# Performance work log

Hardware: AMD Instinct MI355X
Metric: run time of the kernel (lower is better)

Reference implementation:

```python
import jax, jax.numpy as jnp
import numpy as np

IMG_SIZE = 8192
VAR = (0.1, 0.2)          # cfg['variance']
CONF_THRES = 0.9
IOU_THRES = 0.5
TOP_K = 4096              # fixed pre-NMS cap (jit-able replacement for dynamic nonzero/nms sizes)
MIN_SIZES = [[16, 32], [64, 128], [256, 512]]
STEPS = [8, 16, 32]


def _priorbox():
    # Faithful reimplementation of priorbox(min_sizes, steps, clip=False, image_size=(S,S)),
    # vectorized: per cell the anchors for each min_size are interleaved, as in the loop version.
    anchors = []
    for k, step in enumerate(STEPS):
        f = int(np.ceil(IMG_SIZE / step))
        ys, xs = np.meshgrid(np.arange(f, dtype=np.float32), np.arange(f, dtype=np.float32), indexing='ij')
        cx = (xs + 0.5) * step / IMG_SIZE
        cy = (ys + 0.5) * step / IMG_SIZE
        per_size = []
        for m in MIN_SIZES[k]:
            s = np.float32(m / IMG_SIZE)
            per_size.append(np.stack([cx, cy, np.full_like(cx, s), np.full_like(cx, s)], axis=-1))
        anchors.append(np.stack(per_size, axis=2).reshape(-1, 4))  # [f, f, n_sizes, 4] -> [f*f*n_sizes, 4]
    return np.concatenate(anchors, axis=0).astype(np.float32)


def setup_inputs() -> dict:
    key = jax.random.key(0)
    k1, k2, k3 = jax.random.split(key, 3)
    priors = jnp.asarray(_priorbox())                    # [N, 4] (cx, cy, s, s)
    N = priors.shape[0]                                  # 2,752,512
    loc = jax.random.normal(k1, (N, 4), jnp.float32)
    conf = jax.random.uniform(k2, (N, 2), jnp.float32)   # post-softmax class scores
    landm = jax.random.normal(k3, (N, 10), jnp.float32)  # 5 landmark deltas
    return {"loc": loc, "conf": conf, "landm": landm, "priors": priors}


def _decode_boxes(loc, priors):
    # decode(): center-size deltas -> corner boxes (x1, y1, x2, y2)
    xy = priors[:, :2] + loc[:, :2] * VAR[0] * priors[:, 2:]
    wh = priors[:, 2:] * jnp.exp(loc[:, 2:] * VAR[1])
    return jnp.concatenate([xy - 0.5 * wh, xy + 0.5 * wh], axis=1)


def _decode_landm(landm, priors):
    pts = landm.reshape(-1, 5, 2)
    pts = priors[:, None, :2] + pts * VAR[0] * priors[:, None, 2:]
    return pts.reshape(-1, 10)


def _iou_matrix(b):
    # b: [K, 4] corner boxes -> pairwise IoU [K, K]
    area = jnp.clip(b[:, 2] - b[:, 0], 0.0) * jnp.clip(b[:, 3] - b[:, 1], 0.0)
    lt = jnp.maximum(b[:, None, :2], b[None, :, :2])
    rb = jnp.minimum(b[:, None, 2:], b[None, :, 2:])
    wh = jnp.clip(rb - lt, 0.0)
    inter = wh[..., 0] * wh[..., 1]
    return inter / (area[:, None] + area[None, :] - inter + 1e-12)


def reference(loc, conf, landm, priors):
    boxes = _decode_boxes(loc, priors) * IMG_SIZE        # [N, 4]
    landmarks = _decode_landm(landm, priors) * IMG_SIZE  # [N, 10]
    scores = conf[:, 1]                                  # [N]

    # score threshold + fixed-size top-k (jit-able analogue of nonzero(scores > thres))
    masked = jnp.where(scores > CONF_THRES, scores, -jnp.inf)
    top_s, top_i = jax.lax.top_k(masked, TOP_K)          # sorted descending, as torchvision.ops.nms expects
    valid = top_s > CONF_THRES

    b = boxes[top_i]                                     # [K, 4]
    s = scores[top_i]                                    # [K]
    lm = landmarks[top_i]                                # [K, 10]

    # greedy NMS: boxes are score-sorted; suppress later boxes with IoU > thres vs any kept earlier box
    iou = _iou_matrix(b)                                 # [K, K]
    idx = jnp.arange(TOP_K)

    def body(i, keep):
        suppress = keep[i] & (iou[i] > IOU_THRES) & (idx > i)
        return keep & ~suppress

    keep = jax.lax.fori_loop(0, TOP_K, body, valid)

    out = jnp.concatenate([b, s[:, None], lm], axis=1)   # [K, 15] = boxes | score | landmarks
    # zero padded/suppressed rows (fixed-shape stand-in for dynamic boxes[keep])
    return out * keep[:, None].astype(out.dtype)
```

## Files before the change

kernel.cpp:

```cpp
#include <hip/hip_runtime.h>
#include <stdint.h>

typedef unsigned long long u64;
typedef unsigned int u32;

#define CONF_T 0.9f
#define IOU_T 0.5f
#define TOPK 4096
#define CAP 384

#define BINCNT_OFF 0
#define VALIDW_OFF 16384
#define NZW_OFF    16896
#define SELBOX_OFF 32768
#define SELSC_OFF  98304
#define SELLM_OFF  114688
#define MASK_OFF   278528
#define BINSEG_OFF 2375680

__device__ __forceinline__ int score_bin(float s) {
    u32 b = __float_as_uint(s);
    if (b >= 0x3F800000u) return 0;
    int bin = (int)((0x3F800000u - b) >> 9);
    return bin > 4095 ? 4095 : bin;
}

__global__ void k_zero(u32* __restrict__ binCnt, u64* __restrict__ validw,
                       u64* __restrict__ nzw) {
    int i = blockIdx.x * 256 + threadIdx.x;
    binCnt[i] = 0u;
    if (i < 64) { validw[i] = 0ull; nzw[i] = 0ull; }
}

__global__ void __launch_bounds__(256) k_compact(
        const float4* __restrict__ conf4, int N2,
        u32* __restrict__ binCnt, u64* __restrict__ binseg) {
    int stride = gridDim.x * 256;
    for (int i = blockIdx.x * 256 + threadIdx.x; i < N2; i += stride) {
        float4 v = conf4[i];
        if (v.y > CONF_T) {
            int b = score_bin(v.y);
            u32 p = atomicAdd(&binCnt[b], 1u);
            if (p < CAP)
                binseg[(size_t)b * CAP + p] =
                    ((u64)__float_as_uint(v.y) << 32) | (u64)(~(u32)(2 * i));
        }
        if (v.w > CONF_T) {
            int b = score_bin(v.w);
            u32 p = atomicAdd(&binCnt[b], 1u);
            if (p < CAP)
                binseg[(size_t)b * CAP + p] =
                    ((u64)__float_as_uint(v.w) << 32) | (u64)(~(u32)(2 * i + 1));
        }
    }
}

__global__ void __launch_bounds__(256) k_rankscan(
        const float4* __restrict__ loc, const float4* __restrict__ priors,
        const float* __restrict__ landm, const u32* __restrict__ binCnt,
        const u64* __restrict__ binseg,
        float4* __restrict__ selbox, float* __restrict__ selscore,
        float* __restrict__ sellm) {
    __shared__ u32 pref_s[4097];
    __shared__ u32 parts[256];
    __shared__ u32 m_sh;
    int t = threadIdx.x;
    u32 h[16];
    u32 sum = 0;
    #pragma unroll
    for (int i = 0; i < 16; i++) {
        u32 c = binCnt[t * 16 + i];
        h[i] = c > CAP ? CAP : c;
        sum += h[i];
    }
    parts[t] = sum;
    if (t == 0) m_sh = 0u;
    __syncthreads();
    for (int d = 1; d < 256; d <<= 1) {
        u32 add = (t >= d) ? parts[t - d] : 0u;
        __syncthreads();
        parts[t] += add;
        __syncthreads();
    }
    u32 incl = parts[t];
    u32 excl = incl - sum;
    u32 run = excl;
    #pragma unroll
    for (int i = 0; i < 16; i++) { pref_s[t * 16 + i] = run; run += h[i]; }
    if (t == 255) pref_s[4096] = run;
    __syncthreads();
    u32 total = pref_s[4096];
    u32 target = total < TOPK ? total : TOPK;
    if (total > 0 && excl < target && incl >= target) {
        u32 r2 = excl;
        #pragma unroll
        for (int i = 0; i < 16; i++) {
            r2 += h[i];
            if (r2 >= target) { m_sh = r2; break; }
        }
    }
    __syncthreads();
    u32 M = m_sh;
    u32 p = blockIdx.x * 256 + t;
    if (p >= M) {
        if (p < TOPK) {
            selbox[p] = make_float4(0.f, 0.f, 0.f, 0.f);
            selscore[p] = 0.f;
            #pragma unroll
            for (int q = 0; q < 10; q++) sellm[(size_t)p * 10 + q] = 0.f;
        }
        return;
    }
    int lo = 0, hi = 4095;
    while (lo < hi) {
        int mid = (lo + hi + 1) >> 1;
        if (pref_s[mid] <= p) lo = mid; else hi = mid - 1;
    }
    u32 st = pref_s[lo];
    u32 cnt = pref_s[lo + 1] - st;
    const u64* seg = binseg + (size_t)lo * CAP;
    u64 key = seg[p - st];
    u32 rank = st;
    for (u32 j = 0; j < cnt; j++) rank += (seg[j] > key) ? 1u : 0u;
    if (rank >= TOPK) return;
    u32 idx = ~(u32)key;
    float sc = __uint_as_float((u32)(key >> 32));
    float4 L = loc[idx];
    float4 P = priors[idx];
    float cx = P.x + L.x * 0.1f * P.z;
    float cy = P.y + L.y * 0.1f * P.w;
    float wx = P.z * expf(L.z * 0.2f);
    float wy = P.w * expf(L.w * 0.2f);
    float4 bx;
    bx.x = (cx - 0.5f * wx) * 8192.f;
    bx.y = (cy - 0.5f * wy) * 8192.f;
    bx.z = (cx + 0.5f * wx) * 8192.f;
    bx.w = (cy + 0.5f * wy) * 8192.f;
    selbox[rank] = bx;
    selscore[rank] = sc;
    const float* lmr = landm + (size_t)idx * 10;
    float* lmo = sellm + (size_t)rank * 10;
    #pragma unroll
    for (int q = 0; q < 5; q++) {
        float lx = lmr[2 * q], ly = lmr[2 * q + 1];
        lmo[2 * q]     = (P.x + lx * 0.1f * P.z) * 8192.f;
        lmo[2 * q + 1] = (P.y + ly * 0.1f * P.w) * 8192.f;
    }
}

__global__ void __launch_bounds__(256) k_maskout(
        const float4* __restrict__ selbox, const float* __restrict__ selscore,
        const float* __restrict__ sellm,
        u64* __restrict__ mask, u64* __restrict__ validw, u64* __restrict__ nzw,
        float* __restrict__ out) {
    __shared__ float4 sb[TOPK];
    int t = threadIdx.x, b = blockIdx.x;
    for (int i = t; i < TOPK; i += 256) sb[i] = selbox[i];
    __syncthreads();
    int wv = t >> 6, lane = t & 63;
    int rbase = b * 16 + wv * 4;
    float4 r0 = sb[rbase], r1 = sb[rbase + 1], r2 = sb[rbase + 2], r3 = sb[rbase + 3];
    float a0 = fmaxf(r0.z - r0.x, 0.f) * fmaxf(r0.w - r0.y, 0.f);
    float a1 = fmaxf(r1.z - r1.x, 0.f) * fmaxf(r1.w - r1.y, 0.f);
    float a2 = fmaxf(r2.z - r2.x, 0.f) * fmaxf(r2.w - r2.y, 0.f);
    float a3 = fmaxf(r3.z - r3.x, 0.f) * fmaxf(r3.w - r3.y, 0.f);
    u64 w0 = 0, w1 = 0, w2 = 0, w3 = 0;
    for (int w = 0; w < 64; w++) {
        if (w * 64 + 63 <= rbase) continue;
        int j = w * 64 + lane;
        float4 bj = sb[j];
        float aj = fmaxf(bj.z - bj.x, 0.f) * fmaxf(bj.w - bj.y, 0.f);
        #define IOU_BIT(rr, aa, row) ({ \
            float lx = fmaxf(rr.x, bj.x), ly = fmaxf(rr.y, bj.y); \
            float rx = fminf(rr.z, bj.z), ry = fminf(rr.w, bj.w); \
            float inter = fmaxf(rx - lx, 0.f) * fmaxf(ry - ly, 0.f); \
            float iou = inter / (aa + aj - inter + 1e-12f); \
            (j > (row)) && (iou > IOU_T); })
        u64 bb0 = __ballot(IOU_BIT(r0, a0, rbase + 0));
        u64 bb1 = __ballot(IOU_BIT(r1, a1, rbase + 1));
        u64 bb2 = __ballot(IOU_BIT(r2, a2, rbase + 2));
        u64 bb3 = __ballot(IOU_BIT(r3, a3, rbase + 3));
        #undef IOU_BIT
        if (lane == w) { w0 = bb0; w1 = bb1; w2 = bb2; w3 = bb3; }
    }
    mask[(size_t)(rbase + 0) * 64 + lane] = w0;
    mask[(size_t)(rbase + 1) * 64 + lane] = w1;
    mask[(size_t)(rbase + 2) * 64 + lane] = w2;
    mask[(size_t)(rbase + 3) * 64 + lane] = w3;
    u64 nz0 = __ballot(w0 != 0ull), nz1 = __ballot(w1 != 0ull);
    u64 nz2 = __ballot(w2 != 0ull), nz3 = __ballot(w3 != 0ull);
    u64 vb = __ballot(lane < 4 && selscore[rbase + lane] > CONF_T);
    if (lane == 0) {
        int g = rbase >> 6;
        int sh = rbase & 63;
        u64 nzb = (nz0 ? 1ull : 0) | (nz1 ? 2ull : 0) | (nz2 ? 4ull : 0) | (nz3 ? 8ull : 0);
        if (vb)  atomicOr(&validw[g], vb << sh);
        if (nzb) atomicOr(&nzw[g], nzb << sh);
    }
    if (t < 240) {
        int row = b * 16 + t / 15;
        int col = t - (t / 15) * 15;
        const float* sbf = (const float*)selbox;
        float val;
        if (col < 4)       val = sbf[row * 4 + col];
        else if (col == 4) val = selscore[row];
        else               val = sellm[(size_t)row * 10 + (col - 5)];
        out[(size_t)row * 15 + col] = val;
    }
}

__global__ void __launch_bounds__(1024) k_nmszero(
        const u64* __restrict__ mask, const u64* __restrict__ validw_arr,
        const u64* __restrict__ nzw_arr, float* __restrict__ out) {
    __shared__ u64 keep_s[64];
    int tid = threadIdx.x;
    if (tid < 64) {
        int t = tid;
        u64 vw = validw_arr[t];
        u64 nzv = nzw_arr[t];
        u64 sup = 0ull, keepw = 0ull;
        for (int g = 0; g < 64; g++) {
            u64 cur = __shfl(sup, g);
            u64 validg = __shfl(vw, g);
            u64 nzg = __shfl(nzv, g);
            u64 alive = (~cur) & validg;
            if (nzg) {
                u64 intra = mask[(size_t)(g * 64 + t) * 64 + g];
                u64 rem = nzg;
                while (rem) {
                    int bb = __ffsll((long long)rem) - 1;
                    rem &= rem - 1;
                    if ((alive >> bb) & 1ull) {
                        u64 rowb = __shfl(intra, bb);
                        alive &= ~rowb;
                    }
                }
            }
            if (t == g) keepw = alive;
            u64 srem = alive & nzg;
            const u64* mb = mask + (size_t)(g * 64) * 64 + t;
            while (srem) {
                int i0, i1 = -1, i2 = -1, i3 = -1, i4 = -1, i5 = -1, i6 = -1, i7 = -1;
                i0 = __ffsll((long long)srem) - 1; srem &= srem - 1;
                if (srem) { i1 = __ffsll((long long)srem) - 1; srem &= srem - 1;
                if (srem) { i2 = __ffsll((long long)srem) - 1; srem &= srem - 1;
                if (srem) { i3 = __ffsll((long long)srem) - 1; srem &= srem - 1;
                if (srem) { i4 = __ffsll((long long)srem) - 1; srem &= srem - 1;
                if (srem) { i5 = __ffsll((long long)srem) - 1; srem &= srem - 1;
                if (srem) { i6 = __ffsll((long long)srem) - 1; srem &= srem - 1;
                if (srem) { i7 = __ffsll((long long)srem) - 1; srem &= srem - 1; } } } } } } }
                u64 a0 = mb[(size_t)i0 * 64];
                u64 a1 = (i1 >= 0) ? mb[(size_t)i1 * 64] : 0ull;
                u64 a2 = (i2 >= 0) ? mb[(size_t)i2 * 64] : 0ull;
                u64 a3 = (i3 >= 0) ? mb[(size_t)i3 * 64] : 0ull;
                u64 a4 = (i4 >= 0) ? mb[(size_t)i4 * 64] : 0ull;
                u64 a5 = (i5 >= 0) ? mb[(size_t)i5 * 64] : 0ull;
                u64 a6 = (i6 >= 0) ? mb[(size_t)i6 * 64] : 0ull;
                u64 a7 = (i7 >= 0) ? mb[(size_t)i7 * 64] : 0ull;
                sup |= (a0 | a1) | (a2 | a3) | ((a4 | a5) | (a6 | a7));
            }
        }
        keep_s[t] = keepw;
    }
    __syncthreads();
    for (int r = tid; r < TOPK; r += 1024) {
        if (!((keep_s[r >> 6] >> (r & 63)) & 1ull)) {
            float* o = out + (size_t)r * 15;
            #pragma unroll
            for (int q = 0; q < 15; q++) o[q] = 0.f;
        }
    }
}

extern "C" void kernel_launch(void* const* d_in, const int* in_sizes, int n_in,
                              void* d_out, int out_size, void* d_ws, size_t ws_size,
                              hipStream_t stream) {
    const float4* loc    = (const float4*)d_in[0];
    const float4* conf4  = (const float4*)d_in[1];
    const float*  landm  = (const float*)d_in[2];
    const float4* priors = (const float4*)d_in[3];
    float* out = (float*)d_out;
    int N = in_sizes[1] / 2;
    int N2 = N / 2;

    char* ws = (char*)d_ws;
    u32* binCnt   = (u32*)(ws + BINCNT_OFF);
    u64* validw   = (u64*)(ws + VALIDW_OFF);
    u64* nzw      = (u64*)(ws + NZW_OFF);
    float4* selbox = (float4*)(ws + SELBOX_OFF);
    float* selsc   = (float*)(ws + SELSC_OFF);
    float* sellm   = (float*)(ws + SELLM_OFF);
    u64* maskp    = (u64*)(ws + MASK_OFF);
    u64* binseg   = (u64*)(ws + BINSEG_OFF);

    k_zero<<<16, 256, 0, stream>>>(binCnt, validw, nzw);
    k_compact<<<1024, 256, 0, stream>>>(conf4, N2, binCnt, binseg);
    k_rankscan<<<32, 256, 0, stream>>>(loc, priors, landm, binCnt, binseg,
                                       selbox, selsc, sellm);
    k_maskout<<<256, 256, 0, stream>>>(selbox, selsc, sellm, maskp, validw, nzw, out);
    k_nmszero<<<1, 1024, 0, stream>>>(maskp, validw, nzw, out);
}
```

Before: 97.42 us.

## Fuse NMS pipeline into one cooperative persistent kernel with grid syncs

Replaces the five separate kernel launches (zero, compact, rankscan, maskout, nmszero) with a single cooperative kernel of 512 blocks that separates the stages with grid.sync(). The intent is to remove launch gaps and inter-kernel dependency overhead. The IoU mask stage now gives each block 8 rows instead of 16, and the final output is written once, masked by a keep bitmap in global memory, rather than written and then partly zeroed. In exchange it adds five grid-wide barriers and 64 KB of static shared memory per block, which limits occupancy during the memory-bound compaction scan.

```diff
diff --git a/kernel.cpp b/kernel.cpp
--- a/kernel.cpp
+++ b/kernel.cpp
@@ -1,5 +1,8 @@
 #include <hip/hip_runtime.h>
+#include <hip/hip_cooperative_groups.h>
 #include <stdint.h>
+
+namespace cg = cooperative_groups;
 
 typedef unsigned long long u64;
 typedef unsigned int u32;
@@ -8,10 +11,14 @@
 #define IOU_T 0.5f
 #define TOPK 4096
 #define CAP 384
+#define NB 512
+#define NT 256
+#define NTOT (NB * NT)
 
 #define BINCNT_OFF 0
 #define VALIDW_OFF 16384
 #define NZW_OFF    16896
+#define KEEPG_OFF  17408
 #define SELBOX_OFF 32768
 #define SELSC_OFF  98304
 #define SELLM_OFF  114688
@@ -25,199 +32,175 @@
     return bin > 4095 ? 4095 : bin;
 }
 
-__global__ void k_zero(u32* __restrict__ binCnt, u64* __restrict__ validw,
-                       u64* __restrict__ nzw) {
-    int i = blockIdx.x * 256 + threadIdx.x;
-    binCnt[i] = 0u;
-    if (i < 64) { validw[i] = 0ull; nzw[i] = 0ull; }
-}
-
-__global__ void __launch_bounds__(256) k_compact(
+__global__ void __launch_bounds__(NT) mega(
         const float4* __restrict__ conf4, int N2,
-        u32* __restrict__ binCnt, u64* __restrict__ binseg) {
-    int stride = gridDim.x * 256;
-    for (int i = blockIdx.x * 256 + threadIdx.x; i < N2; i += stride) {
+        const float4* __restrict__ loc, const float4* __restrict__ priors,
+        const float* __restrict__ landm,
+        u32* __restrict__ binCnt, u64* __restrict__ binseg,
+        float4* __restrict__ selbox, float* __restrict__ selscore,
+        float* __restrict__ sellm,
+        u64* __restrict__ mask, u64* __restrict__ validw, u64* __restrict__ nzw,
+        u64* __restrict__ keepg, float* __restrict__ out) {
+    cg::grid_group grid = cg::this_grid();
+    __shared__ alignas(16) char smem[65536];
+    int t = threadIdx.x, b = blockIdx.x;
+    int gtid = b * NT + t;
+
+    if (gtid < 4096) binCnt[gtid] = 0u;
+    if (gtid < 64) { validw[gtid] = 0ull; nzw[gtid] = 0ull; }
+    grid.sync();
+
+    for (int i = gtid; i < N2; i += NTOT) {
         float4 v = conf4[i];
         if (v.y > CONF_T) {
-            int b = score_bin(v.y);
-            u32 p = atomicAdd(&binCnt[b], 1u);
+            int bb = score_bin(v.y);
+            u32 p = atomicAdd(&binCnt[bb], 1u);
             if (p < CAP)
-                binseg[(size_t)b * CAP + p] =
+                binseg[(size_t)bb * CAP + p] =
                     ((u64)__float_as_uint(v.y) << 32) | (u64)(~(u32)(2 * i));
         }
         if (v.w > CONF_T) {
-            int b = score_bin(v.w);
-            u32 p = atomicAdd(&binCnt[b], 1u);
+            int bb = score_bin(v.w);
+            u32 p = atomicAdd(&binCnt[bb], 1u);
             if (p < CAP)
-                binseg[(size_t)b * CAP + p] =
+                binseg[(size_t)bb * CAP + p] =
                     ((u64)__float_as_uint(v.w) << 32) | (u64)(~(u32)(2 * i + 1));
         }
     }
-}
-
-__global__ void __launch_bounds__(256) k_rankscan(
-        const float4* __restrict__ loc, const float4* __restrict__ priors,
-        const float* __restrict__ landm, const u32* __restrict__ binCnt,
-        const u64* __restrict__ binseg,
-        float4* __restrict__ selbox, float* __restrict__ selscore,
-        float* __restrict__ sellm) {
-    __shared__ u32 pref_s[4097];
-    __shared__ u32 parts[256];
-    __shared__ u32 m_sh;
-    int t = threadIdx.x;
-    u32 h[16];
-    u32 sum = 0;
-    #pragma unroll
-    for (int i = 0; i < 16; i++) {
-        u32 c = binCnt[t * 16 + i];
-        h[i] = c > CAP ? CAP : c;
-        sum += h[i];
-    }
-    parts[t] = sum;
-    if (t == 0) m_sh = 0u;
-    __syncthreads();
-    for (int d = 1; d < 256; d <<= 1) {
-        u32 add = (t >= d) ? parts[t - d] : 0u;
-        __syncthreads();
-        parts[t] += add;
-        __syncthreads();
-    }
-    u32 incl = parts[t];
-    u32 excl = incl - sum;
-    u32 run = excl;
-    #pragma unroll
-    for (int i = 0; i < 16; i++) { pref_s[t * 16 + i] = run; run += h[i]; }
-    if (t == 255) pref_s[4096] = run;
-    __syncthreads();
-    u32 total = pref_s[4096];
-    u32 target = total < TOPK ? total : TOPK;
-    if (total > 0 && excl < target && incl >= target) {
-        u32 r2 = excl;
+    grid.sync();
+
+    if (b < 32) {
+        u32* pref_s = (u32*)smem;
+        u32* parts  = (u32*)(smem + 16400);
+        u32* m_sh   = (u32*)(smem + 17424);
+        u32 h[16];
+        u32 sum = 0;
         #pragma unroll
         for (int i = 0; i < 16; i++) {
-            r2 += h[i];
-            if (r2 >= target) { m_sh = r2; break; }
-        }
-    }
-    __syncthreads();
-    u32 M = m_sh;
-    u32 p = blockIdx.x * 256 + t;
-    if (p >= M) {
-        if (p < TOPK) {
-            selbox[p] = make_float4(0.f, 0.f, 0.f, 0.f);
-            selscore[p] = 0.f;
+            u32 c = binCnt[t * 16 + i];
+            h[i] = c > CAP ? CAP : c;
+            sum += h[i];
+        }
+        parts[t] = sum;
+        if (t == 0) *m_sh = 0u;
+        __syncthreads();
+        for (int d = 1; d < 256; d <<= 1) {
+            u32 add = (t >= d) ? parts[t - d] : 0u;
+            __syncthreads();
+            parts[t] += add;
+            __syncthreads();
+        }
+        u32 incl = parts[t];
+        u32 excl = incl - sum;
+        u32 run = excl;
+        #pragma unroll
+        for (int i = 0; i < 16; i++) { pref_s[t * 16 + i] = run; run += h[i]; }
+        if (t == 255) pref_s[4096] = run;
+        __syncthreads();
+        u32 total = pref_s[4096];
+        u32 target = total < TOPK ? total : TOPK;
+        if (total > 0 && excl < target && incl >= target) {
+            u32 r2 = excl;
             #pragma unroll
-            for (int q = 0; q < 10; q++) sellm[(size_t)p * 10 + q] = 0.f;
-        }
-        return;
-    }
-    int lo = 0, hi = 4095;
-    while (lo < hi) {
-        int mid = (lo + hi + 1) >> 1;
-        if (pref_s[mid] <= p) lo = mid; else hi = mid - 1;
-    }
-    u32 st = pref_s[lo];
-    u32 cnt = pref_s[lo + 1] - st;
-    const u64* seg = binseg + (size_t)lo * CAP;
-    u64 key = seg[p - st];
-    u32 rank = st;
-    for (u32 j = 0; j < cnt; j++) rank += (seg[j] > key) ? 1u : 0u;
-    if (rank >= TOPK) return;
-    u32 idx = ~(u32)key;
-    float sc = __uint_as_float((u32)(key >> 32));
-    float4 L = loc[idx];
-    float4 P = priors[idx];
-    float cx = P.x + L.x * 0.1f * P.z;
-    float cy = P.y + L.y * 0.1f * P.w;
-    float wx = P.z * expf(L.z * 0.2f);
-    float wy = P.w * expf(L.w * 0.2f);
-    float4 bx;
-    bx.x = (cx - 0.5f * wx) * 8192.f;
-    bx.y = (cy - 0.5f * wy) * 8192.f;
-    bx.z = (cx + 0.5f * wx) * 8192.f;
-    bx.w = (cy + 0.5f * wy) * 8192.f;
-    selbox[rank] = bx;
-    selscore[rank] = sc;
-    const float* lmr = landm + (size_t)idx * 10;
-    float* lmo = sellm + (size_t)rank * 10;
-    #pragma unroll
-    for (int q = 0; q < 5; q++) {
-        float lx = lmr[2 * q], ly = lmr[2 * q + 1];
-        lmo[2 * q]     = (P.x + lx * 0.1f * P.z) * 8192.f;
-        lmo[2 * q + 1] = (P.y + ly * 0.1f * P.w) * 8192.f;
-    }
-}
-
-__global__ void __launch_bounds__(256) k_maskout(
-        const float4* __restrict__ selbox, const float* __restrict__ selscore,
-        const float* __restrict__ sellm,
-        u64* __restrict__ mask, u64* __restrict__ validw, u64* __restrict__ nzw,
-        float* __restrict__ out) {
-    __shared__ float4 sb[TOPK];
-    int t = threadIdx.x, b = blockIdx.x;
-    for (int i = t; i < TOPK; i += 256) sb[i] = selbox[i];
-    __syncthreads();
-    int wv = t >> 6, lane = t & 63;
-    int rbase = b * 16 + wv * 4;
-    float4 r0 = sb[rbase], r1 = sb[rbase + 1], r2 = sb[rbase + 2], r3 = sb[rbase + 3];
-    float a0 = fmaxf(r0.z - r0.x, 0.f) * fmaxf(r0.w - r0.y, 0.f);
-    float a1 = fmaxf(r1.z - r1.x, 0.f) * fmaxf(r1.w - r1.y, 0.f);
-    float a2 = fmaxf(r2.z - r2.x, 0.f) * fmaxf(r2.w - r2.y, 0.f);
-    float a3 = fmaxf(r3.z - r3.x, 0.f) * fmaxf(r3.w - r3.y, 0.f);
-    u64 w0 = 0, w1 = 0, w2 = 0, w3 = 0;
-    for (int w = 0; w < 64; w++) {
-        if (w * 64 + 63 <= rbase) continue;
-        int j = w * 64 + lane;
-        float4 bj = sb[j];
-        float aj = fmaxf(bj.z - bj.x, 0.f) * fmaxf(bj.w - bj.y, 0.f);
-        #define IOU_BIT(rr, aa, row) ({ \
-            float lx = fmaxf(rr.x, bj.x), ly = fmaxf(rr.y, bj.y); \
-            float rx = fminf(rr.z, bj.z), ry = fminf(rr.w, bj.w); \
-            float inter = fmaxf(rx - lx, 0.f) * fmaxf(ry - ly, 0.f); \
-            float iou = inter / (aa + aj - inter + 1e-12f); \
-            (j > (row)) && (iou > IOU_T); })
-        u64 bb0 = __ballot(IOU_BIT(r0, a0, rbase + 0));
-        u64 bb1 = __ballot(IOU_BIT(r1, a1, rbase + 1));
-        u64 bb2 = __ballot(IOU_BIT(r2, a2, rbase + 2));
-        u64 bb3 = __ballot(IOU_BIT(r3, a3, rbase + 3));
-        #undef IOU_BIT
-        if (lane == w) { w0 = bb0; w1 = bb1; w2 = bb2; w3 = bb3; }
-    }
-    mask[(size_t)(rbase + 0) * 64 + lane] = w0;
-    mask[(size_t)(rbase + 1) * 64 + lane] = w1;
-    mask[(size_t)(rbase + 2) * 64 + lane] = w2;
-    mask[(size_t)(rbase + 3) * 64 + lane] = w3;
-    u64 nz0 = __ballot(w0 != 0ull), nz1 = __ballot(w1 != 0ull);
-    u64 nz2 = __ballot(w2 != 0ull), nz3 = __ballot(w3 != 0ull);
-    u64 vb = __ballot(lane < 4 && selscore[rbase + lane] > CONF_T);
-    if (lane == 0) {
-        int g = rbase >> 6;
-        int sh = rbase & 63;
-        u64 nzb = (nz0 ? 1ull : 0) | (nz1 ? 2ull : 0) | (nz2 ? 4ull : 0) | (nz3 ? 8ull : 0);
-        if (vb)  atomicOr(&validw[g], vb << sh);
-        if (nzb) atomicOr(&nzw[g], nzb << sh);
-    }
-    if (t < 240) {
-        int row = b * 16 + t / 15;
-        int col = t - (t / 15) * 15;
-        const float* sbf = (const float*)selbox;
-        float val;
-        if (col < 4)       val = sbf[row * 4 + col];
-        else if (col == 4) val = selscore[row];
-        else               val = sellm[(size_t)row * 10 + (col - 5)];
-        out[(size_t)row * 15 + col] = val;
-    }
-}
-
-__global__ void __launch_bounds__(1024) k_nmszero(
-        const u64* __restrict__ mask, const u64* __restrict__ validw_arr,
-        const u64* __restrict__ nzw_arr, float* __restrict__ out) {
-    __shared__ u64 keep_s[64];
-    int tid = threadIdx.x;
-    if (tid < 64) {
-        int t = tid;
-        u64 vw = validw_arr[t];
-        u64 nzv = nzw_arr[t];
+            for (int i = 0; i < 16; i++) {
+                r2 += h[i];
+                if (r2 >= target) { *m_sh = r2; break; }
+            }
+        }
+        __syncthreads();
+        u32 M = *m_sh;
+        u32 p = (u32)gtid;
+        if (p >= M) {
+            if (p < TOPK) {
+                selbox[p] = make_float4(0.f, 0.f, 0.f, 0.f);
+                selscore[p] = 0.f;
+                #pragma unroll
+                for (int q = 0; q < 10; q++) sellm[(size_t)p * 10 + q] = 0.f;
+            }
+        } else {
+            int lo = 0, hi = 4095;
+            while (lo < hi) {
+                int mid = (lo + hi + 1) >> 1;
+                if (pref_s[mid] <= p) lo = mid; else hi = mid - 1;
+            }
+            u32 st = pref_s[lo];
+            u32 cnt = pref_s[lo + 1] - st;
+            const u64* seg = binseg + (size_t)lo * CAP;
+            u64 key = seg[p - st];
+            u32 rank = st;
+            for (u32 j = 0; j < cnt; j++) rank += (seg[j] > key) ? 1u : 0u;
+            if (rank < TOPK) {
+                u32 idx = ~(u32)key;
+                float sc = __uint_as_float((u32)(key >> 32));
+                float4 L = loc[idx];
+                float4 P = priors[idx];
+                float cx = P.x + L.x * 0.1f * P.z;
+                float cy = P.y + L.y * 0.1f * P.w;
+                float wx = P.z * expf(L.z * 0.2f);
+                float wy = P.w * expf(L.w * 0.2f);
+                float4 bx;
+                bx.x = (cx - 0.5f * wx) * 8192.f;
+                bx.y = (cy - 0.5f * wy) * 8192.f;
+                bx.z = (cx + 0.5f * wx) * 8192.f;
+                bx.w = (cy + 0.5f * wy) * 8192.f;
+                selbox[rank] = bx;
+                selscore[rank] = sc;
+                const float* lmr = landm + (size_t)idx * 10;
+                float* lmo = sellm + (size_t)rank * 10;
+                #pragma unroll
+                for (int q = 0; q < 5; q++) {
+                    float lx = lmr[2 * q], ly = lmr[2 * q + 1];
+                    lmo[2 * q]     = (P.x + lx * 0.1f * P.z) * 8192.f;
+                    lmo[2 * q + 1] = (P.y + ly * 0.1f * P.w) * 8192.f;
+                }
+            }
+        }
+    }
+    grid.sync();
+
+    {
+        float4* sb = (float4*)smem;
+        for (int i = t; i < TOPK; i += NT) sb[i] = selbox[i];
+        __syncthreads();
+        int wv = t >> 6, lane = t & 63;
+        int rbase = b * 8 + wv * 2;
+        float4 r0 = sb[rbase], r1 = sb[rbase + 1];
+        float a0 = fmaxf(r0.z - r0.x, 0.f) * fmaxf(r0.w - r0.y, 0.f);
+        float a1 = fmaxf(r1.z - r1.x, 0.f) * fmaxf(r1.w - r1.y, 0.f);
+        u64 w0 = 0, w1 = 0;
+        for (int w = 0; w < 64; w++) {
+            if (w * 64 + 63 <= rbase) continue;
+            int j = w * 64 + lane;
+            float4 bj = sb[j];
+            float aj = fmaxf(bj.z - bj.x, 0.f) * fmaxf(bj.w - bj.y, 0.f);
+            #define IOU_BIT(rr, aa, row) ({ \
+                float lx = fmaxf(rr.x, bj.x), ly = fmaxf(rr.y, bj.y); \
+                float rx = fminf(rr.z, bj.z), ry = fminf(rr.w, bj.w); \
+                float inter = fmaxf(rx - lx, 0.f) * fmaxf(ry - ly, 0.f); \
+                float iou = inter / (aa + aj - inter + 1e-12f); \
+                (j > (row)) && (iou > IOU_T); })
+            u64 bb0 = __ballot(IOU_BIT(r0, a0, rbase + 0));
+            u64 bb1 = __ballot(IOU_BIT(r1, a1, rbase + 1));
+            #undef IOU_BIT
+            if (lane == w) { w0 = bb0; w1 = bb1; }
+        }
+        mask[(size_t)(rbase + 0) * 64 + lane] = w0;
+        mask[(size_t)(rbase + 1) * 64 + lane] = w1;
+        u64 nz0 = __ballot(w0 != 0ull), nz1 = __ballot(w1 != 0ull);
+        u64 vb = __ballot(lane < 2 && selscore[rbase + lane] > CONF_T);
+        if (lane == 0) {
+            int g = rbase >> 6;
+            int sh = rbase & 63;
+            u64 nzb = (nz0 ? 1ull : 0) | (nz1 ? 2ull : 0);
+            if (vb)  atomicOr(&validw[g], vb << sh);
+            if (nzb) atomicOr(&nzw[g], nzb << sh);
+        }
+    }
+    grid.sync();
+
+    if (b == 0 && t < 64) {
+        u64 vw = validw[t];
+        u64 nzv = nzw[t];
         u64 sup = 0ull, keepw = 0ull;
         for (int g = 0; g < 64; g++) {
             u64 cur = __shfl(sup, g);
@@ -260,15 +243,20 @@
                 sup |= (a0 | a1) | (a2 | a3) | ((a4 | a5) | (a6 | a7));
             }
         }
-        keep_s[t] = keepw;
-    }
-    __syncthreads();
-    for (int r = tid; r < TOPK; r += 1024) {
-        if (!((keep_s[r >> 6] >> (r & 63)) & 1ull)) {
-            float* o = out + (size_t)r * 15;
-            #pragma unroll
-            for (int q = 0; q < 15; q++) o[q] = 0.f;
-        }
+        keepg[t] = keepw;
+    }
+    grid.sync();
+
+    if (gtid < TOPK * 15) {
+        int row = gtid / 15;
+        int col = gtid - row * 15;
+        bool kp = (keepg[row >> 6] >> (row & 63)) & 1ull;
+        const float* sbf = (const float*)selbox;
+        float val;
+        if (col < 4)       val = sbf[row * 4 + col];
+        else if (col == 4) val = selscore[row];
+        else               val = sellm[(size_t)row * 10 + (col - 5)];
+        out[gtid] = kp ? val : 0.f;
     }
 }
 
@@ -287,16 +275,16 @@
     u32* binCnt   = (u32*)(ws + BINCNT_OFF);
     u64* validw   = (u64*)(ws + VALIDW_OFF);
     u64* nzw      = (u64*)(ws + NZW_OFF);
+    u64* keepg    = (u64*)(ws + KEEPG_OFF);
     float4* selbox = (float4*)(ws + SELBOX_OFF);
     float* selsc   = (float*)(ws + SELSC_OFF);
     float* sellm   = (float*)(ws + SELLM_OFF);
     u64* maskp    = (u64*)(ws + MASK_OFF);
     u64* binseg   = (u64*)(ws + BINSEG_OFF);
 
-    k_zero<<<16, 256, 0, stream>>>(binCnt, validw, nzw);
-    k_compact<<<1024, 256, 0, stream>>>(conf4, N2, binCnt, binseg);
-    k_rankscan<<<32, 256, 0, stream>>>(loc, priors, landm, binCnt, binseg,
-                                       selbox, selsc, sellm);
-    k_maskout<<<256, 256, 0, stream>>>(selbox, selsc, sellm, maskp, validw, nzw, out);
-    k_nmszero<<<1, 1024, 0, stream>>>(maskp, validw, nzw, out);
+    void* args[] = { &conf4, &N2, &loc, &priors, &landm,
+                     &binCnt, &binseg, &selbox, &selsc, &sellm,
+                     &maskp, &validw, &nzw, &keepg, &out };
+    hipLaunchCooperativeKernel(reinterpret_cast<void*>(mega),
+                               dim3(NB), dim3(NT), args, 0, stream);
 }
```

Measured after the change: 330.0 us. 3.39x slower.

## Balance IoU mask rows across waves and write output rows in rankscan

Applied to the files above, without the earlier changes.

Each wave in the mask kernel now takes four rows spread across the triangle (wid, 2047-wid, 2048+wid, 4095-wid), so every wave does about the same amount of upper-triangular IoU work. Before, consecutive rows gave early blocks much more work than late ones. The 15-float output rows are now written directly in the rankscan kernel, which removes the gather-and-copy step from the mask kernel. The NMS kernel is launched with 256 threads instead of 1024. The trade-off is that four dependent row passes now run per wave, with less instruction-level parallelism than the previous four-row interleaved ballots.

```diff
diff --git a/kernel.cpp b/kernel.cpp
--- a/kernel.cpp
+++ b/kernel.cpp
@@ -60,7 +60,7 @@
         const float* __restrict__ landm, const u32* __restrict__ binCnt,
         const u64* __restrict__ binseg,
         float4* __restrict__ selbox, float* __restrict__ selscore,
-        float* __restrict__ sellm) {
+        float* __restrict__ sellm, float* __restrict__ out) {
     __shared__ u32 pref_s[4097];
     __shared__ u32 parts[256];
     __shared__ u32 m_sh;
@@ -108,6 +108,9 @@
             selscore[p] = 0.f;
             #pragma unroll
             for (int q = 0; q < 10; q++) sellm[(size_t)p * 10 + q] = 0.f;
+            float* o = out + (size_t)p * 15;
+            #pragma unroll
+            for (int q = 0; q < 15; q++) o[q] = 0.f;
         }
         return;
     }
@@ -140,76 +143,59 @@
     selscore[rank] = sc;
     const float* lmr = landm + (size_t)idx * 10;
     float* lmo = sellm + (size_t)rank * 10;
+    float* o = out + (size_t)rank * 15;
+    o[0] = bx.x; o[1] = bx.y; o[2] = bx.z; o[3] = bx.w; o[4] = sc;
     #pragma unroll
     for (int q = 0; q < 5; q++) {
         float lx = lmr[2 * q], ly = lmr[2 * q + 1];
-        lmo[2 * q]     = (P.x + lx * 0.1f * P.z) * 8192.f;
-        lmo[2 * q + 1] = (P.y + ly * 0.1f * P.w) * 8192.f;
-    }
-}
-
-__global__ void __launch_bounds__(256) k_maskout(
+        float ox = (P.x + lx * 0.1f * P.z) * 8192.f;
+        float oy = (P.y + ly * 0.1f * P.w) * 8192.f;
+        lmo[2 * q] = ox; lmo[2 * q + 1] = oy;
+        o[5 + 2 * q] = ox; o[6 + 2 * q] = oy;
+    }
+}
+
+__global__ void __launch_bounds__(256) k_maskbal(
         const float4* __restrict__ selbox, const float* __restrict__ selscore,
-        const float* __restrict__ sellm,
-        u64* __restrict__ mask, u64* __restrict__ validw, u64* __restrict__ nzw,
-        float* __restrict__ out) {
+        u64* __restrict__ mask, u64* __restrict__ validw, u64* __restrict__ nzw) {
     __shared__ float4 sb[TOPK];
     int t = threadIdx.x, b = blockIdx.x;
     for (int i = t; i < TOPK; i += 256) sb[i] = selbox[i];
     __syncthreads();
     int wv = t >> 6, lane = t & 63;
-    int rbase = b * 16 + wv * 4;
-    float4 r0 = sb[rbase], r1 = sb[rbase + 1], r2 = sb[rbase + 2], r3 = sb[rbase + 3];
-    float a0 = fmaxf(r0.z - r0.x, 0.f) * fmaxf(r0.w - r0.y, 0.f);
-    float a1 = fmaxf(r1.z - r1.x, 0.f) * fmaxf(r1.w - r1.y, 0.f);
-    float a2 = fmaxf(r2.z - r2.x, 0.f) * fmaxf(r2.w - r2.y, 0.f);
-    float a3 = fmaxf(r3.z - r3.x, 0.f) * fmaxf(r3.w - r3.y, 0.f);
-    u64 w0 = 0, w1 = 0, w2 = 0, w3 = 0;
-    for (int w = 0; w < 64; w++) {
-        if (w * 64 + 63 <= rbase) continue;
-        int j = w * 64 + lane;
-        float4 bj = sb[j];
-        float aj = fmaxf(bj.z - bj.x, 0.f) * fmaxf(bj.w - bj.y, 0.f);
-        #define IOU_BIT(rr, aa, row) ({ \
-            float lx = fmaxf(rr.x, bj.x), ly = fmaxf(rr.y, bj.y); \
-            float rx = fminf(rr.z, bj.z), ry = fminf(rr.w, bj.w); \
-            float inter = fmaxf(rx - lx, 0.f) * fmaxf(ry - ly, 0.f); \
-            float iou = inter / (aa + aj - inter + 1e-12f); \
-            (j > (row)) && (iou > IOU_T); })
-        u64 bb0 = __ballot(IOU_BIT(r0, a0, rbase + 0));
-        u64 bb1 = __ballot(IOU_BIT(r1, a1, rbase + 1));
-        u64 bb2 = __ballot(IOU_BIT(r2, a2, rbase + 2));
-        u64 bb3 = __ballot(IOU_BIT(r3, a3, rbase + 3));
-        #undef IOU_BIT
-        if (lane == w) { w0 = bb0; w1 = bb1; w2 = bb2; w3 = bb3; }
-    }
-    mask[(size_t)(rbase + 0) * 64 + lane] = w0;
-    mask[(size_t)(rbase + 1) * 64 + lane] = w1;
-    mask[(size_t)(rbase + 2) * 64 + lane] = w2;
-    mask[(size_t)(rbase + 3) * 64 + lane] = w3;
-    u64 nz0 = __ballot(w0 != 0ull), nz1 = __ballot(w1 != 0ull);
-    u64 nz2 = __ballot(w2 != 0ull), nz3 = __ballot(w3 != 0ull);
-    u64 vb = __ballot(lane < 4 && selscore[rbase + lane] > CONF_T);
-    if (lane == 0) {
-        int g = rbase >> 6;
-        int sh = rbase & 63;
-        u64 nzb = (nz0 ? 1ull : 0) | (nz1 ? 2ull : 0) | (nz2 ? 4ull : 0) | (nz3 ? 8ull : 0);
-        if (vb)  atomicOr(&validw[g], vb << sh);
-        if (nzb) atomicOr(&nzw[g], nzb << sh);
-    }
-    if (t < 240) {
-        int row = b * 16 + t / 15;
-        int col = t - (t / 15) * 15;
-        const float* sbf = (const float*)selbox;
-        float val;
-        if (col < 4)       val = sbf[row * 4 + col];
-        else if (col == 4) val = selscore[row];
-        else               val = sellm[(size_t)row * 10 + (col - 5)];
-        out[(size_t)row * 15 + col] = val;
-    }
-}
-
-__global__ void __launch_bounds__(1024) k_nmszero(
+    int wid = b * 4 + wv;
+    int rows[4] = { wid, 2047 - wid, 2048 + wid, 4095 - wid };
+    #pragma unroll
+    for (int q = 0; q < 4; q++) {
+        int row = rows[q];
+        float4 ri = sb[row];
+        float ai = fmaxf(ri.z - ri.x, 0.f) * fmaxf(ri.w - ri.y, 0.f);
+        u64 myword = 0ull;
+        int wstart = row >> 6;
+        for (int w = wstart; w < 64; w++) {
+            int j = w * 64 + lane;
+            float4 bj = sb[j];
+            float aj = fmaxf(bj.z - bj.x, 0.f) * fmaxf(bj.w - bj.y, 0.f);
+            float lx = fmaxf(ri.x, bj.x), ly = fmaxf(ri.y, bj.y);
+            float rx = fminf(ri.z, bj.z), ry = fminf(ri.w, bj.w);
+            float inter = fmaxf(rx - lx, 0.f) * fmaxf(ry - ly, 0.f);
+            float iou = inter / (ai + aj - inter + 1e-12f);
+            bool pred = (j > row) && (iou > IOU_T);
+            u64 bb = __ballot(pred);
+            if (lane == w) myword = bb;
+        }
+        mask[(size_t)row * 64 + lane] = myword;
+        u64 nzb = __ballot(myword != 0ull);
+        if (lane == 0) {
+            bool v = selscore[row] > CONF_T;
+            int g = row >> 6, sh = row & 63;
+            if (v)   atomicOr(&validw[g], 1ull << sh);
+            if (nzb) atomicOr(&nzw[g], 1ull << sh);
+        }
+    }
+}
+
+__global__ void __launch_bounds__(256) k_nms(
         const u64* __restrict__ mask, const u64* __restrict__ validw_arr,
         const u64* __restrict__ nzw_arr, float* __restrict__ out) {
     __shared__ u64 keep_s[64];
@@ -263,7 +249,7 @@
         keep_s[t] = keepw;
     }
     __syncthreads();
-    for (int r = tid; r < TOPK; r += 1024) {
+    for (int r = tid; r < TOPK; r += 256) {
         if (!((keep_s[r >> 6] >> (r & 63)) & 1ull)) {
             float* o = out + (size_t)r * 15;
             #pragma unroll
@@ -296,7 +282,7 @@
     k_zero<<<16, 256, 0, stream>>>(binCnt, validw, nzw);
     k_compact<<<1024, 256, 0, stream>>>(conf4, N2, binCnt, binseg);
     k_rankscan<<<32, 256, 0, stream>>>(loc, priors, landm, binCnt, binseg,
-                                       selbox, selsc, sellm);
-    k_maskout<<<256, 256, 0, stream>>>(selbox, selsc, sellm, maskp, validw, nzw, out);
-    k_nmszero<<<1, 1024, 0, stream>>>(maskp, validw, nzw, out);
-}
+                                       selbox, selsc, sellm, out);
+    k_maskbal<<<256, 256, 0, stream>>>(selbox, selsc, maskp, validw, nzw);
+    k_nms<<<1, 256, 0, stream>>>(maskp, validw, nzw, out);
+}
```

New measurement: 107.2 us. 1.1x slower.
